# Kernel tuning notes

Hardware: AMD Instinct MI355X
Metric: run time of the kernel (lower is better)

Reference implementation:

```python
import jax, jax.numpy as jnp
import numpy as np

K = 2
CAPACITY_FACTOR = 1.25


def setup_inputs() -> dict:
    key = jax.random.key(0)
    ks = jax.random.split(key, 5)
    B, T, D, F, E = 4, 2048, 1024, 4096, 8
    x = jax.random.normal(ks[0], (B, T, D), dtype=jnp.float32)
    w_gate = jax.random.normal(ks[1], (E, D), dtype=jnp.float32) * (1.0 / np.sqrt(D))
    W1 = jax.random.normal(ks[2], (E, F, D), dtype=jnp.float32) * np.sqrt(2.0 / (D + F))
    b1 = jnp.zeros((E, F), dtype=jnp.float32)
    W2 = jax.random.normal(ks[3], (E, D, F), dtype=jnp.float32) * np.sqrt(2.0 / (D + F))
    b2 = jnp.zeros((E, D), dtype=jnp.float32)
    return {"x": x, "w_gate": w_gate, "W1": W1, "b1": b1, "W2": W2, "b2": b2}


def reference(x, w_gate, W1, b1, W2, b2):
    B, T, D = x.shape
    E = w_gate.shape[0]
    S = B * T
    C = int(CAPACITY_FACTOR * S * K / E)  # per-expert capacity
    tokens = x.reshape(S, D)

    # --- routing (fp32 softmax, top-k) ---
    logits = tokens @ w_gate.T                      # [S, E]
    probs = jax.nn.softmax(logits, axis=-1)         # [S, E]
    topk_vals, topk_idx = jax.lax.top_k(probs, K)   # [S, K]

    e_flat = topk_idx.reshape(-1)                   # [S*K] expert id per assignment
    g_flat = topk_vals.reshape(-1)                  # [S*K] gate value
    t_flat = jnp.repeat(jnp.arange(S), K)           # [S*K] source token index

    # --- capacity: position of each assignment within its expert (arrival order) ---
    onehot = jax.nn.one_hot(e_flat, E, dtype=jnp.int32)       # [S*K, E]
    pos = jnp.sum(jnp.cumsum(onehot, axis=0) * onehot, axis=-1) - 1  # [S*K]
    keep = pos < C

    # --- dispatch into [E, C, D] buffer (over-capacity assignments dropped) ---
    buf = jnp.zeros((E, C, D), dtype=tokens.dtype).at[e_flat, pos].set(
        tokens[t_flat], mode="drop")

    # --- grouped expert FFN: fc2(gelu(fc1(x))) + x  (exact gelu, as torch F.gelu) ---
    h = jax.nn.gelu(jnp.einsum("ecd,efd->ecf", buf, W1) + b1[:, None, :],
                    approximate=False)              # [E, C, F]
    expert_out = jnp.einsum("ecf,edf->ecd", h, W2) + b2[:, None, :] + buf  # [E, C, D]

    # --- combine: scatter-add gate-weighted expert outputs back to tokens ---
    gathered = expert_out[e_flat, jnp.clip(pos, 0, C - 1)]    # [S*K, D]
    w = jnp.where(keep, g_flat, 0.0)[:, None]
    y = jnp.zeros((S, D), dtype=tokens.dtype).at[t_flat].add(w * gathered)

    # --- load-balancing aux loss ---
    importance = probs.mean(axis=0)                            # [E]
    counts = jnp.zeros((E,), dtype=probs.dtype).at[e_flat].add(1.0)
    load = counts / S
    aux_loss = E * jnp.sum(importance * load)

    return y.reshape(B, T, D), aux_loss
```

## Files before the change

### kernel.cpp

```cpp
#include <hip/hip_runtime.h>
#include <hip/hip_bf16.h>
#include <math.h>
#include <stdint.h>

#define S_TOK 8192
#define D_DIM 1024
#define F_DIM 4096
#define E_EXP 8
#define C_CAP 2560

typedef __bf16 bf16x8_t __attribute__((ext_vector_type(8)));
typedef __bf16 bf16x4_t __attribute__((ext_vector_type(4)));
typedef float f32x4_t __attribute__((ext_vector_type(4)));

__device__ __forceinline__ void async_copy16(const void* g, void* l) {
  __builtin_amdgcn_global_load_lds(
      (const __attribute__((address_space(1))) unsigned int*)g,
      (__attribute__((address_space(3))) unsigned int*)l, 16, 0, 0);
}

__global__ __launch_bounds__(256) void routing_kernel(
    const float* __restrict__ x, const float* __restrict__ wg,
    __bf16* __restrict__ x_bf, int* __restrict__ asg_e, float* __restrict__ asg_g,
    float* __restrict__ imp_sum)
{
  __shared__ float s_imp[E_EXP];
  const int tid = threadIdx.x, lane = tid & 63, w = tid >> 6;
  if (tid < E_EXP) s_imp[tid] = 0.f;
  __syncthreads();
  const int t = blockIdx.x * 4 + w;

  const float4* xp = (const float4*)(x + (size_t)t * D_DIM);
  float4 xv[4];
#pragma unroll
  for (int j = 0; j < 4; j++) xv[j] = xp[lane + 64 * j];

#pragma unroll
  for (int j = 0; j < 4; j++) {
    bf16x4_t o;
    o[0] = (__bf16)xv[j].x; o[1] = (__bf16)xv[j].y;
    o[2] = (__bf16)xv[j].z; o[3] = (__bf16)xv[j].w;
    *(bf16x4_t*)(x_bf + (size_t)t * D_DIM + (size_t)(lane + 64 * j) * 4) = o;
  }

  float acc[E_EXP];
#pragma unroll
  for (int e = 0; e < E_EXP; e++) acc[e] = 0.f;
#pragma unroll
  for (int e = 0; e < E_EXP; e++) {
    const float4* wp = (const float4*)(wg + (size_t)e * D_DIM);
#pragma unroll
    for (int j = 0; j < 4; j++) {
      const float4 wv = wp[lane + 64 * j];
      acc[e] += xv[j].x * wv.x + xv[j].y * wv.y + xv[j].z * wv.z + xv[j].w * wv.w;
    }
  }
#pragma unroll
  for (int e = 0; e < E_EXP; e++)
    for (int off = 32; off > 0; off >>= 1) acc[e] += __shfl_xor(acc[e], off);

  if (lane == 0) {
    float m = acc[0];
#pragma unroll
    for (int e = 1; e < E_EXP; e++) m = fmaxf(m, acc[e]);
    float p[E_EXP], s = 0.f;
#pragma unroll
    for (int e = 0; e < E_EXP; e++) { p[e] = expf(acc[e] - m); s += p[e]; }
    const float inv = 1.f / s;
#pragma unroll
    for (int e = 0; e < E_EXP; e++) p[e] *= inv;
    int e0 = 0; float v0 = p[0];
#pragma unroll
    for (int e = 1; e < E_EXP; e++) if (p[e] > v0) { v0 = p[e]; e0 = e; }
    int e1 = -1; float v1 = -1.f;
#pragma unroll
    for (int e = 0; e < E_EXP; e++) if (e != e0 && p[e] > v1) { v1 = p[e]; e1 = e; }
    asg_e[2 * t] = e0; asg_g[2 * t] = v0;
    asg_e[2 * t + 1] = e1; asg_g[2 * t + 1] = v1;
#pragma unroll
    for (int e = 0; e < E_EXP; e++) atomicAdd(&s_imp[e], p[e]);
  }
  __syncthreads();
  if (tid < E_EXP) atomicAdd(&imp_sum[tid], s_imp[tid]);
}

__global__ __launch_bounds__(256) void cvt_kernel(const float* __restrict__ src,
                                                  __bf16* __restrict__ dst, int n4)
{
  const int stride = gridDim.x * blockDim.x;
  for (int i = blockIdx.x * blockDim.x + threadIdx.x; i < n4; i += stride) {
    const float4 v = ((const float4*)src)[i];
    bf16x4_t o;
    o[0] = (__bf16)v.x; o[1] = (__bf16)v.y; o[2] = (__bf16)v.z; o[3] = (__bf16)v.w;
    ((bf16x4_t*)dst)[i] = o;
  }
}

__global__ __launch_bounds__(256) void positions_kernel(
    const int* __restrict__ asg_e, const float* __restrict__ asg_g,
    const float* __restrict__ imp_sum, int* __restrict__ slot_token,
    float* __restrict__ slot_gate, int* __restrict__ cnt_g, float* __restrict__ aux_out)
{
  __shared__ int lcnt[E_EXP * 256];
  __shared__ int tot[E_EXP];
  const int tid = threadIdx.x;
  for (int i = tid; i < E_EXP * C_CAP; i += 256) slot_token[i] = -1;
  int cnt[E_EXP];
#pragma unroll
  for (int e = 0; e < E_EXP; e++) cnt[e] = 0;
  const int a0 = tid * 64;
  for (int j = 0; j < 64; j++) cnt[asg_e[a0 + j]]++;
#pragma unroll
  for (int e = 0; e < E_EXP; e++) lcnt[e * 256 + tid] = cnt[e];
  __syncthreads();
  if (tid < E_EXP) {
    int run = 0;
    for (int i = 0; i < 256; i++) { const int v = lcnt[tid * 256 + i]; lcnt[tid * 256 + i] = run; run += v; }
    tot[tid] = run;
    cnt_g[tid] = run;
  }
  __syncthreads();
  int base[E_EXP];
#pragma unroll
  for (int e = 0; e < E_EXP; e++) base[e] = lcnt[e * 256 + tid];
  for (int j = 0; j < 64; j++) {
    const int a = a0 + j;
    const int e = asg_e[a];
    const int pp = base[e]++;
    if (pp < C_CAP) { slot_token[e * C_CAP + pp] = a >> 1; slot_gate[e * C_CAP + pp] = asg_g[a]; }
  }
  if (tid == 0) {
    float aux = 0.f;
#pragma unroll
    for (int e = 0; e < E_EXP; e++) aux += imp_sum[e] * (float)tot[e];
    aux_out[0] = (float)E_EXP * aux / ((float)S_TOK * (float)S_TOK);
  }
}

template <int MODE>
__global__ __launch_bounds__(256, 3) void moe_gemm(
    const __bf16* __restrict__ A, const __bf16* __restrict__ Bw,
    const float* __restrict__ bias, const int* __restrict__ slot_token,
    const float* __restrict__ slot_gate, const float* __restrict__ xres,
    const int* __restrict__ cnt, __bf16* __restrict__ Hout, float* __restrict__ y,
    int MT, int NT, int N, int K)
{
  const int ntiles = gridDim.x;
  const int xcd = blockIdx.x & 7, slot = blockIdx.x >> 3;
  const int tile = xcd * (ntiles >> 3) + slot;
  const int e = tile / (MT * NT);
  const int t = tile % (MT * NT);
  const int grp = t / (4 * NT), rem = t % (4 * NT);
  const int mt = grp * 4 + (rem & 3), nt = rem >> 2;
  const int m0 = mt * 128, n0 = nt * 128;
  if (m0 >= cnt[e]) return;

  const int tid = threadIdx.x, lane = tid & 63, w = tid >> 6;
  const int wm = w >> 1, wn = w & 1;

  __shared__ __align__(16) unsigned short sA[128 * 64];
  __shared__ __align__(16) unsigned short sB[128 * 64];

  const int rstage = lane >> 3;
  const int cstage = (lane & 7) ^ rstage;

  const char* gA[4];
  const char* gB[4];
  void* lA[4];
  void* lB[4];
#pragma unroll
  for (int i = 0; i < 4; i++) {
    const int rowA = w * 32 + i * 8 + rstage;
    size_t arow;
    if (MODE == 0) {
      int tok = slot_token[e * C_CAP + m0 + rowA];
      if (tok < 0) tok = 0;
      arow = (size_t)tok * (size_t)K;
    } else {
      arow = ((size_t)(e * C_CAP + m0 + rowA)) * (size_t)K;
    }
    gA[i] = (const char*)(A + arow) + cstage * 16;
    lA[i] = (void*)&sA[(w * 32 + i * 8) * 64];
    const int rowB = w * 32 + i * 8 + rstage;
    const size_t brow = ((size_t)(e * N + n0 + rowB)) * (size_t)K;
    gB[i] = (const char*)(Bw + brow) + cstage * 16;
    lB[i] = (void*)&sB[(w * 32 + i * 8) * 64];
  }

  f32x4_t acc[4][4];
#pragma unroll
  for (int mi = 0; mi < 4; mi++)
#pragma unroll
    for (int ni = 0; ni < 4; ni++) acc[mi][ni] = (f32x4_t){0.f, 0.f, 0.f, 0.f};

  const int fr = lane & 15;
  const int fq = lane >> 4;
  for (int k0 = 0; k0 < K; k0 += 64) {
    const size_t koff = (size_t)k0 * 2;
    __syncthreads();
#pragma unroll
    for (int i = 0; i < 4; i++) async_copy16(gA[i] + koff, lA[i]);
#pragma unroll
    for (int i = 0; i < 4; i++) async_copy16(gB[i] + koff, lB[i]);
    __syncthreads();
#pragma unroll
    for (int kk = 0; kk < 2; kk++) {
      bf16x8_t af[4], bfv[4];
#pragma unroll
      for (int mi = 0; mi < 4; mi++) {
        const int row = wm * 64 + mi * 16 + fr;
        const int chk = (kk * 4 + fq) ^ (row & 7);
        af[mi] = *(const bf16x8_t*)&sA[row * 64 + chk * 8];
      }
#pragma unroll
      for (int ni = 0; ni < 4; ni++) {
        const int row = wn * 64 + ni * 16 + fr;
        const int chk = (kk * 4 + fq) ^ (row & 7);
        bfv[ni] = *(const bf16x8_t*)&sB[row * 64 + chk * 8];
      }
#pragma unroll
      for (int mi = 0; mi < 4; mi++)
#pragma unroll
        for (int ni = 0; ni < 4; ni++)
          acc[mi][ni] = __builtin_amdgcn_mfma_f32_16x16x32_bf16(af[mi], bfv[ni], acc[mi][ni], 0, 0, 0);
    }
  }

  const int col_lo = lane & 15;
  const int row_hi = (lane >> 4) * 4;
  if (MODE == 0) {
#pragma unroll
    for (int ni = 0; ni < 4; ni++) {
      const int gcol = n0 + wn * 64 + ni * 16 + col_lo;
      const float bv = bias[e * N + gcol];
#pragma unroll
      for (int mi = 0; mi < 4; mi++) {
#pragma unroll
        for (int r = 0; r < 4; r++) {
          const int grow = m0 + wm * 64 + mi * 16 + row_hi + r;
          const float v = acc[mi][ni][r] + bv;
          const float gl = 0.5f * v * (1.0f + erff(v * 0.70710678118654752f));
          Hout[((size_t)(e * C_CAP + grow)) * (size_t)N + gcol] = (__bf16)gl;
        }
      }
    }
  } else {
#pragma unroll
    for (int mi = 0; mi < 4; mi++) {
#pragma unroll
      for (int r = 0; r < 4; r++) {
        const int slot = e * C_CAP + m0 + wm * 64 + mi * 16 + row_hi + r;
        const int tok = slot_token[slot];
        if (tok < 0) continue;
        const float g = slot_gate[slot];
        const size_t trow = (size_t)tok * (size_t)N;
#pragma unroll
        for (int ni = 0; ni < 4; ni++) {
          const int gcol = n0 + wn * 64 + ni * 16 + col_lo;
          const float v = acc[mi][ni][r] + bias[e * N + gcol] + xres[trow + gcol];
          atomicAdd(&y[trow + gcol], g * v);
        }
      }
    }
  }
}

extern "C" void kernel_launch(void* const* d_in, const int* in_sizes, int n_in,
                              void* d_out, int out_size, void* d_ws, size_t ws_size,
                              hipStream_t stream) {
  const float* x  = (const float*)d_in[0];
  const float* wg = (const float*)d_in[1];
  const float* W1 = (const float*)d_in[2];
  const float* b1 = (const float*)d_in[3];
  const float* W2 = (const float*)d_in[4];
  const float* b2 = (const float*)d_in[5];
  float* y = (float*)d_out;

  char* p = (char*)d_ws;
  __bf16* x_bf = (__bf16*)p;    p += (size_t)S_TOK * D_DIM * 2;
  __bf16* w1_bf = (__bf16*)p;   p += (size_t)E_EXP * F_DIM * D_DIM * 2;
  __bf16* w2_bf = (__bf16*)p;   p += (size_t)E_EXP * F_DIM * D_DIM * 2;
  __bf16* Hbuf = (__bf16*)p;    p += (size_t)E_EXP * C_CAP * F_DIM * 2;
  int* slot_token = (int*)p;    p += (size_t)E_EXP * C_CAP * 4;
  float* slot_gate = (float*)p; p += (size_t)E_EXP * C_CAP * 4;
  int* asg_e = (int*)p;         p += (size_t)S_TOK * 2 * 4;
  float* asg_g = (float*)p;     p += (size_t)S_TOK * 2 * 4;
  float* imp_sum = (float*)p;   p += 64;
  int* cnt_g = (int*)p;         p += 64;

  hipMemsetAsync(d_out, 0, ((size_t)S_TOK * D_DIM + 1) * sizeof(float), stream);
  hipMemsetAsync(imp_sum, 0, E_EXP * sizeof(float), stream);

  routing_kernel<<<S_TOK / 4, 256, 0, stream>>>(x, wg, x_bf, asg_e, asg_g, imp_sum);
  cvt_kernel<<<2048, 256, 0, stream>>>(W1, w1_bf, E_EXP * F_DIM * D_DIM / 4);
  cvt_kernel<<<2048, 256, 0, stream>>>(W2, w2_bf, E_EXP * F_DIM * D_DIM / 4);
  positions_kernel<<<1, 256, 0, stream>>>(asg_e, asg_g, imp_sum, slot_token, slot_gate,
                                          cnt_g, y + (size_t)S_TOK * D_DIM);
  moe_gemm<0><<<E_EXP * 20 * 32, 256, 0, stream>>>(x_bf, w1_bf, b1, slot_token, nullptr, nullptr,
                                                   cnt_g, Hbuf, nullptr, 20, 32, F_DIM, D_DIM);
  moe_gemm<1><<<E_EXP * 20 * 8, 256, 0, stream>>>(Hbuf, w2_bf, b2, slot_token, slot_gate, x,
                                                  cnt_g, nullptr, y, 20, 8, D_DIM, F_DIM);
}
```

Baseline: 885.7 us.

## Double-buffer MoE GEMM with 512-thread larger tiles and phased MFMA schedule

Rewrites the expert GEMM to use 512-thread blocks with 256x256 (FC1) and 128x256 (FC2) tiles, double-buffered LDS, and prefetching of the next K-tile via async global-to-LDS copies overlapped with four MFMA phases, using explicit vmcnt waits and s_setprio. The aim is to hide global load latency and raise data reuse per tile. It also moves the slot_token init to a memset and makes the positions kernel use register-friendly per-expert counters instead of dynamically indexed arrays. The costs are more LDS and register pressure, fewer blocks per CU, and fragile manual waitcnt and barrier ordering.

```diff
diff --git a/kernel.cpp b/kernel.cpp
--- a/kernel.cpp
+++ b/kernel.cpp
@@ -104,12 +104,15 @@
   __shared__ int lcnt[E_EXP * 256];
   __shared__ int tot[E_EXP];
   const int tid = threadIdx.x;
-  for (int i = tid; i < E_EXP * C_CAP; i += 256) slot_token[i] = -1;
   int cnt[E_EXP];
 #pragma unroll
   for (int e = 0; e < E_EXP; e++) cnt[e] = 0;
   const int a0 = tid * 64;
-  for (int j = 0; j < 64; j++) cnt[asg_e[a0 + j]]++;
+  for (int j = 0; j < 64; j++) {
+    const int ae = asg_e[a0 + j];
+#pragma unroll
+    for (int e = 0; e < E_EXP; e++) cnt[e] += (ae == e) ? 1 : 0;
+  }
 #pragma unroll
   for (int e = 0; e < E_EXP; e++) lcnt[e * 256 + tid] = cnt[e];
   __syncthreads();
@@ -125,9 +128,13 @@
   for (int e = 0; e < E_EXP; e++) base[e] = lcnt[e * 256 + tid];
   for (int j = 0; j < 64; j++) {
     const int a = a0 + j;
-    const int e = asg_e[a];
-    const int pp = base[e]++;
-    if (pp < C_CAP) { slot_token[e * C_CAP + pp] = a >> 1; slot_gate[e * C_CAP + pp] = asg_g[a]; }
+    const int ae = asg_e[a];
+    int pp = 0;
+#pragma unroll
+    for (int e = 0; e < E_EXP; e++) {
+      if (ae == e) { pp = base[e]; base[e] = pp + 1; }
+    }
+    if (pp < C_CAP) { slot_token[ae * C_CAP + pp] = a >> 1; slot_gate[ae * C_CAP + pp] = asg_g[a]; }
   }
   if (tid == 0) {
     float aux = 0.f;
@@ -137,40 +144,50 @@
   }
 }
 
+#define WAIT_VM4  asm volatile("s_waitcnt vmcnt(4)" ::: "memory")
+#define WAIT_VM2  asm volatile("s_waitcnt vmcnt(2)" ::: "memory")
+#define WAIT_VM0  asm volatile("s_waitcnt vmcnt(0)" ::: "memory")
+#define WAIT_LGKM asm volatile("s_waitcnt lgkmcnt(0)" ::: "memory")
+
 template <int MODE>
-__global__ __launch_bounds__(256, 3) void moe_gemm(
+__global__ __launch_bounds__(512, 2) void moe_gemm(
     const __bf16* __restrict__ A, const __bf16* __restrict__ Bw,
     const float* __restrict__ bias, const int* __restrict__ slot_token,
     const float* __restrict__ slot_gate, const float* __restrict__ xres,
     const int* __restrict__ cnt, __bf16* __restrict__ Hout, float* __restrict__ y,
-    int MT, int NT, int N, int K)
+    int MT, int NTT, int N, int K)
 {
+  constexpr int BM = (MODE == 0) ? 256 : 128;
+  constexpr int MFRAG = BM / 32;
+  constexpr int MH = MFRAG / 2;
+  constexpr int ALOADS = BM / 64;
+
   const int ntiles = gridDim.x;
-  const int xcd = blockIdx.x & 7, slot = blockIdx.x >> 3;
-  const int tile = xcd * (ntiles >> 3) + slot;
-  const int e = tile / (MT * NT);
-  const int t = tile % (MT * NT);
-  const int grp = t / (4 * NT), rem = t % (4 * NT);
-  const int mt = grp * 4 + (rem & 3), nt = rem >> 2;
-  const int m0 = mt * 128, n0 = nt * 128;
+  const int xcd = blockIdx.x & 7, bslot = blockIdx.x >> 3;
+  const int tile = xcd * (ntiles >> 3) + bslot;
+  const int e = tile / (MT * NTT);
+  const int t_ = tile % (MT * NTT);
+  const int grp = t_ / (2 * NTT), rem = t_ % (2 * NTT);
+  const int mt = grp * 2 + (rem & 1), nt = rem >> 1;
+  const int m0 = mt * BM, n0 = nt * 256;
   if (m0 >= cnt[e]) return;
 
   const int tid = threadIdx.x, lane = tid & 63, w = tid >> 6;
-  const int wm = w >> 1, wn = w & 1;
-
-  __shared__ __align__(16) unsigned short sA[128 * 64];
-  __shared__ __align__(16) unsigned short sB[128 * 64];
+  const int wm = w >> 2, wn = w & 3;
+
+  __shared__ __align__(16) unsigned short sA[2][BM][64];
+  __shared__ __align__(16) unsigned short sB[2][256][64];
 
   const int rstage = lane >> 3;
   const int cstage = (lane & 7) ^ rstage;
-
-  const char* gA[4];
+  const int wArow = w * (BM / 8);
+  const int wBrow = w * 32;
+
+  const char* gA[ALOADS];
   const char* gB[4];
-  void* lA[4];
-  void* lB[4];
-#pragma unroll
-  for (int i = 0; i < 4; i++) {
-    const int rowA = w * 32 + i * 8 + rstage;
+#pragma unroll
+  for (int i = 0; i < ALOADS; i++) {
+    const int rowA = wArow + i * 8 + rstage;
     size_t arow;
     if (MODE == 0) {
       int tok = slot_token[e * C_CAP + m0 + rowA];
@@ -180,50 +197,116 @@
       arow = ((size_t)(e * C_CAP + m0 + rowA)) * (size_t)K;
     }
     gA[i] = (const char*)(A + arow) + cstage * 16;
-    lA[i] = (void*)&sA[(w * 32 + i * 8) * 64];
-    const int rowB = w * 32 + i * 8 + rstage;
-    const size_t brow = ((size_t)(e * N + n0 + rowB)) * (size_t)K;
-    gB[i] = (const char*)(Bw + brow) + cstage * 16;
-    lB[i] = (void*)&sB[(w * 32 + i * 8) * 64];
-  }
-
-  f32x4_t acc[4][4];
-#pragma unroll
-  for (int mi = 0; mi < 4; mi++)
+  }
+#pragma unroll
+  for (int i = 0; i < 4; i++) {
+    const int rowB = wBrow + i * 8 + rstage;
+    gB[i] = (const char*)(Bw + ((size_t)(e * N + n0 + rowB)) * (size_t)K) + cstage * 16;
+  }
+
+#define STAGE_A(buf, kt)                                                        \
+  _Pragma("unroll")                                                             \
+  for (int i_ = 0; i_ < ALOADS; i_++)                                           \
+    async_copy16(gA[i_] + (size_t)(kt) * 128, (void*)&sA[buf][wArow + i_ * 8][0]);
+#define STAGE_B(buf, kt)                                                        \
+  _Pragma("unroll")                                                             \
+  for (int i_ = 0; i_ < 4; i_++)                                                \
+    async_copy16(gB[i_] + (size_t)(kt) * 128, (void*)&sB[buf][wBrow + i_ * 8][0]);
+
+  f32x4_t acc[MFRAG][4];
+#pragma unroll
+  for (int mi = 0; mi < MFRAG; mi++)
 #pragma unroll
     for (int ni = 0; ni < 4; ni++) acc[mi][ni] = (f32x4_t){0.f, 0.f, 0.f, 0.f};
 
   const int fr = lane & 15;
   const int fq = lane >> 4;
-  for (int k0 = 0; k0 < K; k0 += 64) {
-    const size_t koff = (size_t)k0 * 2;
-    __syncthreads();
-#pragma unroll
-    for (int i = 0; i < 4; i++) async_copy16(gA[i] + koff, lA[i]);
-#pragma unroll
-    for (int i = 0; i < 4; i++) async_copy16(gB[i] + koff, lB[i]);
-    __syncthreads();
-#pragma unroll
-    for (int kk = 0; kk < 2; kk++) {
-      bf16x8_t af[4], bfv[4];
-#pragma unroll
-      for (int mi = 0; mi < 4; mi++) {
-        const int row = wm * 64 + mi * 16 + fr;
-        const int chk = (kk * 4 + fq) ^ (row & 7);
-        af[mi] = *(const bf16x8_t*)&sA[row * 64 + chk * 8];
+  const int NTILES = K >> 6;
+
+#define DS_A(PM)                                                                \
+  _Pragma("unroll")                                                             \
+  for (int i_ = 0; i_ < MH; i_++) {                                             \
+    _Pragma("unroll")                                                           \
+    for (int kk_ = 0; kk_ < 2; kk_++) {                                         \
+      const int row_ = wm * (BM / 2) + ((PM) * MH + i_) * 16 + fr;              \
+      const int chk_ = (kk_ * 4 + fq) ^ (row_ & 7);                             \
+      af[i_][kk_] = *(const bf16x8_t*)&sA[cur][row_][chk_ * 8];                 \
+    }                                                                           \
+  }
+#define DS_B(PN)                                                                \
+  _Pragma("unroll")                                                             \
+  for (int i_ = 0; i_ < 2; i_++) {                                              \
+    _Pragma("unroll")                                                           \
+    for (int kk_ = 0; kk_ < 2; kk_++) {                                         \
+      const int row_ = wn * 64 + ((PN) * 2 + i_) * 16 + fr;                     \
+      const int chk_ = (kk_ * 4 + fq) ^ (row_ & 7);                             \
+      bfr[i_][kk_] = *(const bf16x8_t*)&sB[cur][row_][chk_ * 8];                \
+    }                                                                           \
+  }
+#define MFMA_PH(PM, PN)                                                         \
+  _Pragma("unroll")                                                             \
+  for (int kk_ = 0; kk_ < 2; kk_++) {                                           \
+    _Pragma("unroll")                                                           \
+    for (int i_ = 0; i_ < MH; i_++) {                                           \
+      _Pragma("unroll")                                                         \
+      for (int j_ = 0; j_ < 2; j_++)                                            \
+        acc[(PM) * MH + i_][(PN) * 2 + j_] = __builtin_amdgcn_mfma_f32_16x16x32_bf16( \
+            af[i_][kk_], bfr[j_][kk_], acc[(PM) * MH + i_][(PN) * 2 + j_], 0, 0, 0); \
+    }                                                                           \
+  }
+
+  STAGE_A(0, 0);
+  STAGE_B(0, 0);
+  if (NTILES > 1) {
+    STAGE_A(1, 1);
+    if constexpr (ALOADS == 4) { WAIT_VM4; } else { WAIT_VM2; }
+  } else {
+    WAIT_VM0;
+  }
+  __builtin_amdgcn_s_barrier();
+
+  for (int t = 0; t < NTILES; ++t) {
+    const int cur = t & 1;
+    bf16x8_t af[MH][2], bfr[2][2];
+    DS_A(0);
+    DS_B(0);
+    if (t + 1 < NTILES) STAGE_B(cur ^ 1, t + 1);
+    __builtin_amdgcn_s_barrier();
+    WAIT_LGKM;
+    __builtin_amdgcn_s_setprio(1);
+    MFMA_PH(0, 0);
+    __builtin_amdgcn_s_setprio(0);
+    __builtin_amdgcn_s_barrier();
+    DS_B(1);
+    __builtin_amdgcn_s_barrier();
+    WAIT_LGKM;
+    __builtin_amdgcn_s_setprio(1);
+    MFMA_PH(0, 1);
+    __builtin_amdgcn_s_setprio(0);
+    __builtin_amdgcn_s_barrier();
+    DS_A(1);
+    DS_B(0);
+    __builtin_amdgcn_s_barrier();
+    WAIT_LGKM;
+    __builtin_amdgcn_s_setprio(1);
+    MFMA_PH(1, 0);
+    __builtin_amdgcn_s_setprio(0);
+    __builtin_amdgcn_s_barrier();
+    DS_B(1);
+    if (t + 2 < NTILES) STAGE_A(cur, t + 2);
+    __builtin_amdgcn_s_barrier();
+    WAIT_LGKM;
+    __builtin_amdgcn_s_setprio(1);
+    MFMA_PH(1, 1);
+    __builtin_amdgcn_s_setprio(0);
+    if (t + 1 < NTILES) {
+      if (t + 2 < NTILES) {
+        if constexpr (ALOADS == 4) { WAIT_VM4; } else { WAIT_VM2; }
+      } else {
+        WAIT_VM0;
       }
-#pragma unroll
-      for (int ni = 0; ni < 4; ni++) {
-        const int row = wn * 64 + ni * 16 + fr;
-        const int chk = (kk * 4 + fq) ^ (row & 7);
-        bfv[ni] = *(const bf16x8_t*)&sB[row * 64 + chk * 8];
-      }
-#pragma unroll
-      for (int mi = 0; mi < 4; mi++)
-#pragma unroll
-        for (int ni = 0; ni < 4; ni++)
-          acc[mi][ni] = __builtin_amdgcn_mfma_f32_16x16x32_bf16(af[mi], bfv[ni], acc[mi][ni], 0, 0, 0);
-    }
+    }
+    __builtin_amdgcn_s_barrier();
   }
 
   const int col_lo = lane & 15;
@@ -234,10 +317,10 @@
       const int gcol = n0 + wn * 64 + ni * 16 + col_lo;
       const float bv = bias[e * N + gcol];
 #pragma unroll
-      for (int mi = 0; mi < 4; mi++) {
+      for (int mi = 0; mi < MFRAG; mi++) {
 #pragma unroll
         for (int r = 0; r < 4; r++) {
-          const int grow = m0 + wm * 64 + mi * 16 + row_hi + r;
+          const int grow = m0 + wm * (BM / 2) + mi * 16 + row_hi + r;
           const float v = acc[mi][ni][r] + bv;
           const float gl = 0.5f * v * (1.0f + erff(v * 0.70710678118654752f));
           Hout[((size_t)(e * C_CAP + grow)) * (size_t)N + gcol] = (__bf16)gl;
@@ -246,13 +329,13 @@
     }
   } else {
 #pragma unroll
-    for (int mi = 0; mi < 4; mi++) {
+    for (int mi = 0; mi < MFRAG; mi++) {
 #pragma unroll
       for (int r = 0; r < 4; r++) {
-        const int slot = e * C_CAP + m0 + wm * 64 + mi * 16 + row_hi + r;
-        const int tok = slot_token[slot];
+        const int slotI = e * C_CAP + m0 + wm * (BM / 2) + mi * 16 + row_hi + r;
+        const int tok = slot_token[slotI];
         if (tok < 0) continue;
-        const float g = slot_gate[slot];
+        const float g = slot_gate[slotI];
         const size_t trow = (size_t)tok * (size_t)N;
 #pragma unroll
         for (int ni = 0; ni < 4; ni++) {
@@ -263,6 +346,11 @@
       }
     }
   }
+#undef STAGE_A
+#undef STAGE_B
+#undef DS_A
+#undef DS_B
+#undef MFMA_PH
 }
 
 extern "C" void kernel_launch(void* const* d_in, const int* in_sizes, int n_in,
@@ -290,14 +378,17 @@
 
   hipMemsetAsync(d_out, 0, ((size_t)S_TOK * D_DIM + 1) * sizeof(float), stream);
   hipMemsetAsync(imp_sum, 0, E_EXP * sizeof(float), stream);
+  hipMemsetAsync(slot_token, 0xFF, (size_t)E_EXP * C_CAP * sizeof(int), stream);
 
   routing_kernel<<<S_TOK / 4, 256, 0, stream>>>(x, wg, x_bf, asg_e, asg_g, imp_sum);
   cvt_kernel<<<2048, 256, 0, stream>>>(W1, w1_bf, E_EXP * F_DIM * D_DIM / 4);
   cvt_kernel<<<2048, 256, 0, stream>>>(W2, w2_bf, E_EXP * F_DIM * D_DIM / 4);
   positions_kernel<<<1, 256, 0, stream>>>(asg_e, asg_g, imp_sum, slot_token, slot_gate,
                                           cnt_g, y + (size_t)S_TOK * D_DIM);
-  moe_gemm<0><<<E_EXP * 20 * 32, 256, 0, stream>>>(x_bf, w1_bf, b1, slot_token, nullptr, nullptr,
-                                                   cnt_g, Hbuf, nullptr, 20, 32, F_DIM, D_DIM);
-  moe_gemm<1><<<E_EXP * 20 * 8, 256, 0, stream>>>(Hbuf, w2_bf, b2, slot_token, slot_gate, x,
-                                                  cnt_g, nullptr, y, 20, 8, D_DIM, F_DIM);
-}
+  moe_gemm<0><<<E_EXP * 10 * 16, 512, 0, stream>>>(x_bf, w1_bf, b1, slot_token, nullptr,
+                                                   nullptr, cnt_g, Hbuf, nullptr,
+                                                   10, 16, F_DIM, D_DIM);
+  moe_gemm<1><<<E_EXP * 20 * 4, 512, 0, stream>>>(Hbuf, w2_bf, b2, slot_token, slot_gate,
+                                                  x, cnt_g, nullptr, y,
+                                                  20, 4, D_DIM, F_DIM);
+}
```

Result: slower. 1.108 ms (+25.1%).

## Double-buffer GEMM LDS tiles and fuse weight conversions into one kernel

Applied to the files above, without the earlier changes.

The MoE GEMM now keeps two LDS buffers. It prefetches the next K tile with async global-to-LDS loads while MFMAs run on the current one, and needs one barrier per tile instead of two. It also raises MFMA priority and lowers launch bounds to 2 blocks per SM to make room for the doubled shared memory. Separately, the two weight conversions are merged into one launch, slot_token initialisation moves to a memset, and positions counting avoids dynamic register indexing. The cost is lower occupancy and more LDS per block.

```diff
diff --git a/kernel.cpp b/kernel.cpp
--- a/kernel.cpp
+++ b/kernel.cpp
@@ -84,15 +84,18 @@
   if (tid < E_EXP) atomicAdd(&imp_sum[tid], s_imp[tid]);
 }
 
-__global__ __launch_bounds__(256) void cvt_kernel(const float* __restrict__ src,
-                                                  __bf16* __restrict__ dst, int n4)
+__global__ __launch_bounds__(256) void cvt2_kernel(
+    const float* __restrict__ s1, const float* __restrict__ s2,
+    __bf16* __restrict__ d1, __bf16* __restrict__ d2, int n4each)
 {
   const int stride = gridDim.x * blockDim.x;
-  for (int i = blockIdx.x * blockDim.x + threadIdx.x; i < n4; i += stride) {
-    const float4 v = ((const float4*)src)[i];
+  for (int i = blockIdx.x * blockDim.x + threadIdx.x; i < 2 * n4each; i += stride) {
+    const int half = (i >= n4each);
+    const int j = half ? (i - n4each) : i;
+    const float4 v = half ? ((const float4*)s2)[j] : ((const float4*)s1)[j];
     bf16x4_t o;
     o[0] = (__bf16)v.x; o[1] = (__bf16)v.y; o[2] = (__bf16)v.z; o[3] = (__bf16)v.w;
-    ((bf16x4_t*)dst)[i] = o;
+    if (half) ((bf16x4_t*)d2)[j] = o; else ((bf16x4_t*)d1)[j] = o;
   }
 }
 
@@ -104,12 +107,15 @@
   __shared__ int lcnt[E_EXP * 256];
   __shared__ int tot[E_EXP];
   const int tid = threadIdx.x;
-  for (int i = tid; i < E_EXP * C_CAP; i += 256) slot_token[i] = -1;
   int cnt[E_EXP];
 #pragma unroll
   for (int e = 0; e < E_EXP; e++) cnt[e] = 0;
   const int a0 = tid * 64;
-  for (int j = 0; j < 64; j++) cnt[asg_e[a0 + j]]++;
+  for (int j = 0; j < 64; j++) {
+    const int ae = asg_e[a0 + j];
+#pragma unroll
+    for (int e = 0; e < E_EXP; e++) cnt[e] += (ae == e) ? 1 : 0;
+  }
 #pragma unroll
   for (int e = 0; e < E_EXP; e++) lcnt[e * 256 + tid] = cnt[e];
   __syncthreads();
@@ -125,9 +131,13 @@
   for (int e = 0; e < E_EXP; e++) base[e] = lcnt[e * 256 + tid];
   for (int j = 0; j < 64; j++) {
     const int a = a0 + j;
-    const int e = asg_e[a];
-    const int pp = base[e]++;
-    if (pp < C_CAP) { slot_token[e * C_CAP + pp] = a >> 1; slot_gate[e * C_CAP + pp] = asg_g[a]; }
+    const int ae = asg_e[a];
+    int pp = 0;
+#pragma unroll
+    for (int e = 0; e < E_EXP; e++) {
+      if (ae == e) { pp = base[e]; base[e] = pp + 1; }
+    }
+    if (pp < C_CAP) { slot_token[ae * C_CAP + pp] = a >> 1; slot_gate[ae * C_CAP + pp] = asg_g[a]; }
   }
   if (tid == 0) {
     float aux = 0.f;
@@ -137,8 +147,10 @@
   }
 }
 
+#define WAIT_VM0 asm volatile("s_waitcnt vmcnt(0)" ::: "memory")
+
 template <int MODE>
-__global__ __launch_bounds__(256, 3) void moe_gemm(
+__global__ __launch_bounds__(256, 2) void moe_gemm(
     const __bf16* __restrict__ A, const __bf16* __restrict__ Bw,
     const float* __restrict__ bias, const int* __restrict__ slot_token,
     const float* __restrict__ slot_gate, const float* __restrict__ xres,
@@ -149,8 +161,8 @@
   const int xcd = blockIdx.x & 7, slot = blockIdx.x >> 3;
   const int tile = xcd * (ntiles >> 3) + slot;
   const int e = tile / (MT * NT);
-  const int t = tile % (MT * NT);
-  const int grp = t / (4 * NT), rem = t % (4 * NT);
+  const int t_ = tile % (MT * NT);
+  const int grp = t_ / (4 * NT), rem = t_ % (4 * NT);
   const int mt = grp * 4 + (rem & 3), nt = rem >> 2;
   const int m0 = mt * 128, n0 = nt * 128;
   if (m0 >= cnt[e]) return;
@@ -158,16 +170,14 @@
   const int tid = threadIdx.x, lane = tid & 63, w = tid >> 6;
   const int wm = w >> 1, wn = w & 1;
 
-  __shared__ __align__(16) unsigned short sA[128 * 64];
-  __shared__ __align__(16) unsigned short sB[128 * 64];
+  __shared__ __align__(16) unsigned short sA[2][128][64];
+  __shared__ __align__(16) unsigned short sB[2][128][64];
 
   const int rstage = lane >> 3;
   const int cstage = (lane & 7) ^ rstage;
 
   const char* gA[4];
   const char* gB[4];
-  void* lA[4];
-  void* lB[4];
 #pragma unroll
   for (int i = 0; i < 4; i++) {
     const int rowA = w * 32 + i * 8 + rstage;
@@ -180,12 +190,20 @@
       arow = ((size_t)(e * C_CAP + m0 + rowA)) * (size_t)K;
     }
     gA[i] = (const char*)(A + arow) + cstage * 16;
-    lA[i] = (void*)&sA[(w * 32 + i * 8) * 64];
     const int rowB = w * 32 + i * 8 + rstage;
     const size_t brow = ((size_t)(e * N + n0 + rowB)) * (size_t)K;
     gB[i] = (const char*)(Bw + brow) + cstage * 16;
-    lB[i] = (void*)&sB[(w * 32 + i * 8) * 64];
-  }
+  }
+
+#define STAGE(BUF, kt) do {                                                         \
+    const size_t koff_ = (size_t)(kt) * 128;                                        \
+    _Pragma("unroll")                                                               \
+    for (int i_ = 0; i_ < 4; i_++)                                                  \
+      async_copy16(gA[i_] + koff_, (void*)&sA[BUF][w * 32 + i_ * 8][0]);            \
+    _Pragma("unroll")                                                               \
+    for (int i_ = 0; i_ < 4; i_++)                                                  \
+      async_copy16(gB[i_] + koff_, (void*)&sB[BUF][w * 32 + i_ * 8][0]);            \
+  } while (0)
 
   f32x4_t acc[4][4];
 #pragma unroll
@@ -195,34 +213,50 @@
 
   const int fr = lane & 15;
   const int fq = lane >> 4;
-  for (int k0 = 0; k0 < K; k0 += 64) {
-    const size_t koff = (size_t)k0 * 2;
-    __syncthreads();
-#pragma unroll
-    for (int i = 0; i < 4; i++) async_copy16(gA[i] + koff, lA[i]);
-#pragma unroll
-    for (int i = 0; i < 4; i++) async_copy16(gB[i] + koff, lB[i]);
-    __syncthreads();
-#pragma unroll
-    for (int kk = 0; kk < 2; kk++) {
-      bf16x8_t af[4], bfv[4];
-#pragma unroll
-      for (int mi = 0; mi < 4; mi++) {
-        const int row = wm * 64 + mi * 16 + fr;
-        const int chk = (kk * 4 + fq) ^ (row & 7);
-        af[mi] = *(const bf16x8_t*)&sA[row * 64 + chk * 8];
-      }
-#pragma unroll
-      for (int ni = 0; ni < 4; ni++) {
-        const int row = wn * 64 + ni * 16 + fr;
-        const int chk = (kk * 4 + fq) ^ (row & 7);
-        bfv[ni] = *(const bf16x8_t*)&sB[row * 64 + chk * 8];
-      }
-#pragma unroll
-      for (int mi = 0; mi < 4; mi++)
-#pragma unroll
-        for (int ni = 0; ni < 4; ni++)
-          acc[mi][ni] = __builtin_amdgcn_mfma_f32_16x16x32_bf16(af[mi], bfv[ni], acc[mi][ni], 0, 0, 0);
+
+#define COMPUTE(BUF)                                                                \
+  _Pragma("unroll")                                                                 \
+  for (int kk = 0; kk < 2; kk++) {                                                  \
+    bf16x8_t af[4], bfv[4];                                                         \
+    _Pragma("unroll")                                                               \
+    for (int mi = 0; mi < 4; mi++) {                                                \
+      const int row = wm * 64 + mi * 16 + fr;                                       \
+      const int chk = (kk * 4 + fq) ^ (row & 7);                                    \
+      af[mi] = *(const bf16x8_t*)&sA[BUF][row][chk * 8];                            \
+    }                                                                               \
+    _Pragma("unroll")                                                               \
+    for (int ni = 0; ni < 4; ni++) {                                                \
+      const int row = wn * 64 + ni * 16 + fr;                                       \
+      const int chk = (kk * 4 + fq) ^ (row & 7);                                    \
+      bfv[ni] = *(const bf16x8_t*)&sB[BUF][row][chk * 8];                           \
+    }                                                                               \
+    __builtin_amdgcn_s_setprio(1);                                                  \
+    _Pragma("unroll")                                                               \
+    for (int mi = 0; mi < 4; mi++)                                                  \
+      _Pragma("unroll")                                                             \
+      for (int ni = 0; ni < 4; ni++)                                                \
+        acc[mi][ni] = __builtin_amdgcn_mfma_f32_16x16x32_bf16(af[mi], bfv[ni],      \
+                                                              acc[mi][ni], 0, 0, 0);\
+    __builtin_amdgcn_s_setprio(0);                                                  \
+  }
+
+  const int NTILES = K >> 6;
+  STAGE(0, 0);
+  WAIT_VM0;
+  __builtin_amdgcn_s_barrier();
+
+  for (int t = 0; t < NTILES; t += 2) {
+    STAGE(1, t + 1);
+    COMPUTE(0);
+    WAIT_VM0;
+    __builtin_amdgcn_s_barrier();
+    if (t + 2 < NTILES) {
+      STAGE(0, t + 2);
+      COMPUTE(1);
+      WAIT_VM0;
+      __builtin_amdgcn_s_barrier();
+    } else {
+      COMPUTE(1);
     }
   }
 
@@ -249,10 +283,10 @@
     for (int mi = 0; mi < 4; mi++) {
 #pragma unroll
       for (int r = 0; r < 4; r++) {
-        const int slot = e * C_CAP + m0 + wm * 64 + mi * 16 + row_hi + r;
-        const int tok = slot_token[slot];
+        const int slotI = e * C_CAP + m0 + wm * 64 + mi * 16 + row_hi + r;
+        const int tok = slot_token[slotI];
         if (tok < 0) continue;
-        const float g = slot_gate[slot];
+        const float g = slot_gate[slotI];
         const size_t trow = (size_t)tok * (size_t)N;
 #pragma unroll
         for (int ni = 0; ni < 4; ni++) {
@@ -263,6 +297,8 @@
       }
     }
   }
+#undef STAGE
+#undef COMPUTE
 }
 
 extern "C" void kernel_launch(void* const* d_in, const int* in_sizes, int n_in,
@@ -290,14 +326,16 @@
 
   hipMemsetAsync(d_out, 0, ((size_t)S_TOK * D_DIM + 1) * sizeof(float), stream);
   hipMemsetAsync(imp_sum, 0, E_EXP * sizeof(float), stream);
+  hipMemsetAsync(slot_token, 0xFF, (size_t)E_EXP * C_CAP * sizeof(int), stream);
 
   routing_kernel<<<S_TOK / 4, 256, 0, stream>>>(x, wg, x_bf, asg_e, asg_g, imp_sum);
-  cvt_kernel<<<2048, 256, 0, stream>>>(W1, w1_bf, E_EXP * F_DIM * D_DIM / 4);
-  cvt_kernel<<<2048, 256, 0, stream>>>(W2, w2_bf, E_EXP * F_DIM * D_DIM / 4);
+  cvt2_kernel<<<4096, 256, 0, stream>>>(W1, W2, w1_bf, w2_bf, E_EXP * F_DIM * D_DIM / 4);
   positions_kernel<<<1, 256, 0, stream>>>(asg_e, asg_g, imp_sum, slot_token, slot_gate,
                                           cnt_g, y + (size_t)S_TOK * D_DIM);
-  moe_gemm<0><<<E_EXP * 20 * 32, 256, 0, stream>>>(x_bf, w1_bf, b1, slot_token, nullptr, nullptr,
-                                                   cnt_g, Hbuf, nullptr, 20, 32, F_DIM, D_DIM);
-  moe_gemm<1><<<E_EXP * 20 * 8, 256, 0, stream>>>(Hbuf, w2_bf, b2, slot_token, slot_gate, x,
-                                                  cnt_g, nullptr, y, 20, 8, D_DIM, F_DIM);
-}
+  moe_gemm<0><<<E_EXP * 20 * 32, 256, 0, stream>>>(x_bf, w1_bf, b1, slot_token, nullptr,
+                                                   nullptr, cnt_g, Hbuf, nullptr,
+                                                   20, 32, F_DIM, D_DIM);
+  moe_gemm<1><<<E_EXP * 20 * 8, 256, 0, stream>>>(Hbuf, w2_bf, b2, slot_token, slot_gate,
+                                                  x, cnt_g, nullptr, y,
+                                                  20, 8, D_DIM, F_DIM);
+}
```

After: 1.033 ms. +16.6%, slower.
